# Kernel optimization log

Hardware: AMD Instinct MI355X
Metric: run time of the kernel (lower is better)

The kernel has to match this reference:

```python
import jax, jax.numpy as jnp
import numpy as np

M, K, L, OUT = 16, 64, 6, 128
IN_CH = 2 + 1 + 1 + 1 + 4 * L  # 29
HID_IN = 128 * 2 + 4           # 260


def setup_inputs() -> dict:
    key = jax.random.key(0)
    ks = jax.random.split(key, 5)
    N = 2_000_000
    P = jax.random.normal(ks[0], (N, 2), jnp.float32) * 2.0
    def lin(k, i, o):
        return jax.random.normal(k, (i, o), jnp.float32) / np.float32(np.sqrt(i))
    return {
        'P': P,
        'W1': lin(ks[1], IN_CH, 64), 'b1': jnp.zeros((64,), jnp.float32),
        'W2': lin(ks[2], 64, 128),   'b2': jnp.zeros((128,), jnp.float32),
        'W3': lin(ks[3], HID_IN, 128), 'b3': jnp.zeros((128,), jnp.float32),
        'W4': lin(ks[4], 128, OUT),  'b4': jnp.zeros((OUT,), jnp.float32),
    }


def _fps(P, m):
    # furthest point sampling, seeded at index 0 (standard convention)
    N = P.shape[0]
    def step(carry, _):
        min_d, last_idx = carry
        last = P[last_idx]
        d = jnp.sum((P - last) ** 2, axis=-1)          # [N]
        min_d = jnp.minimum(min_d, d)
        nxt = jnp.argmax(min_d)
        return (min_d, nxt), last_idx
    init = (jnp.full((N,), jnp.finfo(jnp.float32).max, jnp.float32), jnp.int32(0))
    (_, _), idxs = jax.lax.scan(step, init, None, length=m)
    return idxs  # [m] int


def _gelu(x):
    return jax.nn.gelu(x, approximate=False)  # torch nn.GELU default = erf


def reference(P, W1, b1, W2, b2, W3, b3, W4, b4):
    c_idx = jax.lax.stop_gradient(_fps(P, M))
    C = P[c_idx]                                       # [M,2]
    # brute-force kNN: expanded squared distance avoids [M,N,2] intermediate
    Ps = jax.lax.stop_gradient(P)
    Cs = jax.lax.stop_gradient(C)
    d2 = (jnp.sum(Ps ** 2, -1)[None, :]
          - 2.0 * Cs @ Ps.T
          + jnp.sum(Cs ** 2, -1)[:, None])             # [M,N]
    _, nidx = jax.lax.top_k(-d2, K)                    # [M,K]
    patch = P[nidx]                                    # [M,K,2]
    delta = patch - C[:, None, :]                      # [M,K,2]
    r = jnp.linalg.norm(delta, axis=-1, keepdims=True) # [M,K,1]
    theta = jnp.arctan2(delta[..., 1:2], delta[..., 0:1])
    freqs = (2.0 ** jnp.arange(L)).astype(jnp.float32) # [L]
    ang = delta[..., None, :] * freqs[:, None]         # [M,K,L,2]
    ff = jnp.concatenate([jnp.sin(ang), jnp.cos(ang)], -1).reshape(M, K, 4 * L)
    per_pt = jnp.concatenate([delta, r, jnp.sin(theta), jnp.cos(theta), ff], -1)  # [M,K,29]
    h = _gelu(per_pt @ W1 + b1)
    h = _gelu(h @ W2 + b2)                             # [M,K,128]
    h_max = h.max(axis=1)
    h_mean = h.mean(axis=1)
    rr = r[..., 0]                                     # [M,K]
    stats = jnp.stack([rr.mean(1), rr.max(1), rr.min(1), rr.std(1, ddof=1)], -1)  # [M,4]
    z = jnp.concatenate([h_max, h_mean, stats], -1)    # [M,260]
    F = _gelu(z @ W3 + b3) @ W4 + b4                   # [M,OUT]
    return F, C
```

## Files before the change

### kernel.cpp

```cpp
#include <hip/hip_runtime.h>
#include <math.h>

#define MCENT 16
#define KNN   64
#define NBINS 512
#define CAP   7936
#define FPSB  512
#define FPST  256

__device__ __forceinline__ float gelu_f(float x){
    return 0.5f * x * (1.0f + erff(x * 0.70710678118654752440f));
}

__global__ void init_kernel(unsigned int* __restrict__ ghist,
                            unsigned int* __restrict__ cnt){
    const int T = gridDim.x * blockDim.x;
    int t = blockIdx.x * blockDim.x + threadIdx.x;
    for (int i = t; i < MCENT*NBINS; i += T) ghist[i] = 0u;
    if (t < MCENT) cnt[t] = 0u;
}

__global__ __launch_bounds__(FPST) void fps_step(
    const float* __restrict__ P, int N,
    float* __restrict__ min_d,
    unsigned long long* __restrict__ partials,
    int k,
    float* __restrict__ cxy,
    float* __restrict__ outC)
{
    const int lane = threadIdx.x & 63;
    const int wid  = threadIdx.x >> 6;
    __shared__ unsigned long long wred[FPST/64];
    __shared__ int s_cur;

    int cur = 0;
    if (k > 0){
        unsigned long long pb = 0ULL;
        for (int i = threadIdx.x; i < FPSB; i += FPST){
            unsigned long long v = partials[(k-1)*FPSB + i];
            if (v > pb) pb = v;
        }
#pragma unroll
        for (int off = 32; off > 0; off >>= 1){
            unsigned long long o = __shfl_xor(pb, off, 64);
            if (o > pb) pb = o;
        }
        if (lane == 0) wred[wid] = pb;
        __syncthreads();
        if (threadIdx.x == 0){
            unsigned long long b = wred[0];
#pragma unroll
            for (int w = 1; w < FPST/64; ++w) if (wred[w] > b) b = wred[w];
            s_cur = (int)(0xFFFFFFFFu - (unsigned)(b & 0xFFFFFFFFu));
        }
        __syncthreads();
        cur = s_cur;
    }

    if (blockIdx.x == 0 && threadIdx.x == 0){
        float cx = P[2*cur], cy = P[2*cur+1];
        cxy[2*k] = cx; cxy[2*k+1] = cy;
        outC[2*k] = cx; outC[2*k+1] = cy;
    }
    if (k >= MCENT-1) return;

    const float cx = P[2*cur], cy = P[2*cur+1];
    unsigned long long bk = 0ULL;
    const int T = gridDim.x * FPST;
    for (int g = blockIdx.x*FPST + threadIdx.x; g < N; g += T){
        float2 p = ((const float2*)P)[g];
        float dx = __fsub_rn(p.x, cx);
        float dy = __fsub_rn(p.y, cy);
        float d  = __fadd_rn(__fmul_rn(dx,dx), __fmul_rn(dy,dy));
        float nm = (k == 0) ? d : fminf(min_d[g], d);
        min_d[g] = nm;
        unsigned long long key =
            ((unsigned long long)__float_as_uint(nm) << 32)
            | (unsigned long long)(0xFFFFFFFFu - (unsigned)g);
        if (key > bk) bk = key;
    }
#pragma unroll
    for (int off = 32; off > 0; off >>= 1){
        unsigned long long o = __shfl_xor(bk, off, 64);
        if (o > bk) bk = o;
    }
    if (lane == 0) wred[wid] = bk;
    __syncthreads();
    if (threadIdx.x == 0){
        unsigned long long b = wred[0];
#pragma unroll
        for (int w = 1; w < FPST/64; ++w) if (wred[w] > b) b = wred[w];
        partials[k*FPSB + blockIdx.x] = b;
    }
}

__global__ __launch_bounds__(256) void hist_kernel(
    const float* __restrict__ P, int N,
    const float* __restrict__ cxy,
    unsigned int* __restrict__ ghist)
{
    __shared__ unsigned int h[MCENT*NBINS];
    __shared__ float scx[MCENT], scy[MCENT], scs2[MCENT];
    for (int i = threadIdx.x; i < MCENT*NBINS; i += blockDim.x) h[i] = 0u;
    if (threadIdx.x < MCENT){
        float a = cxy[2*threadIdx.x], b = cxy[2*threadIdx.x+1];
        scx[threadIdx.x] = a; scy[threadIdx.x] = b;
        scs2[threadIdx.x] = __fadd_rn(__fmul_rn(a,a), __fmul_rn(b,b));
    }
    __syncthreads();
    const int T = gridDim.x * blockDim.x;
    for (int g = blockIdx.x*blockDim.x + threadIdx.x; g < N; g += T){
        float2 p = ((const float2*)P)[g];
        float x = p.x, y = p.y;
        float ps2 = __fadd_rn(__fmul_rn(x,x), __fmul_rn(y,y));
#pragma unroll
        for (int m = 0; m < MCENT; ++m){
            float dot = __fadd_rn(__fmul_rn(scx[m],x), __fmul_rn(scy[m],y));
            float d2  = __fadd_rn(__fsub_rn(ps2, __fmul_rn(2.0f,dot)), scs2[m]);
            unsigned bin = __float_as_uint(fmaxf(d2, 0.0f)) >> 22;
            atomicAdd(&h[m*NBINS + bin], 1u);
        }
    }
    __syncthreads();
    for (int i = threadIdx.x; i < MCENT*NBINS; i += blockDim.x){
        unsigned v = h[i];
        if (v) atomicAdd(&ghist[i], v);
    }
}

__global__ void thr_kernel(const unsigned int* __restrict__ ghist,
                           float* __restrict__ thr){
    int m = threadIdx.x;
    if (m < MCENT){
        unsigned cum = 0; int B = NBINS-1;
        for (int b = 0; b < NBINS; ++b){
            cum += ghist[m*NBINS + b];
            if (cum >= KNN){ B = b; break; }
        }
        thr[m] = __uint_as_float((unsigned)(B+1) << 22);
    }
}

__global__ __launch_bounds__(256) void collect_kernel(
    const float* __restrict__ P, int N,
    const float* __restrict__ cxy,
    const float* __restrict__ thr,
    unsigned int* __restrict__ cnt,
    float* __restrict__ cd2,
    int* __restrict__ cidx)
{
    __shared__ float scx[MCENT], scy[MCENT], scs2[MCENT], sth[MCENT];
    if (threadIdx.x < MCENT){
        float a = cxy[2*threadIdx.x], b = cxy[2*threadIdx.x+1];
        scx[threadIdx.x]=a; scy[threadIdx.x]=b;
        scs2[threadIdx.x]=__fadd_rn(__fmul_rn(a,a),__fmul_rn(b,b));
        sth[threadIdx.x]=thr[threadIdx.x];
    }
    __syncthreads();
    const int T = gridDim.x*blockDim.x;
    for (int g = blockIdx.x*blockDim.x + threadIdx.x; g < N; g += T){
        float2 p = ((const float2*)P)[g];
        float x = p.x, y = p.y;
        float ps2=__fadd_rn(__fmul_rn(x,x),__fmul_rn(y,y));
#pragma unroll
        for (int m=0;m<MCENT;++m){
            float dot=__fadd_rn(__fmul_rn(scx[m],x),__fmul_rn(scy[m],y));
            float d2=__fadd_rn(__fsub_rn(ps2,__fmul_rn(2.0f,dot)),scs2[m]);
            if (fmaxf(d2,0.0f) < sth[m]){
                unsigned p2 = atomicAdd(&cnt[m], 1u);
                if (p2 < CAP){ cd2[m*CAP+p2]=d2; cidx[m*CAP+p2]=g; }
            }
        }
    }
}

__global__ __launch_bounds__(256) void select_kernel(
    const unsigned int* __restrict__ cnt,
    const float* __restrict__ cd2,
    const int* __restrict__ cidx,
    int* __restrict__ nbr)
{
    const int m = blockIdx.x;
    __shared__ unsigned long long keys[CAP];
    unsigned c = cnt[m]; if (c > CAP) c = CAP;
    for (int i = threadIdx.x; i < (int)c; i += 256){
        unsigned u = __float_as_uint(cd2[m*CAP+i]);
        u = (u & 0x80000000u) ? ~u : (u | 0x80000000u);
        keys[i] = ((unsigned long long)u << 32)
                | (unsigned long long)(unsigned)cidx[m*CAP+i];
    }
    __syncthreads();
    for (int i = threadIdx.x; i < (int)c; i += 256){
        unsigned long long ki = keys[i];
        int rank = 0;
        for (int j = 0; j < (int)c; ++j) rank += (keys[j] < ki);
        if (rank < KNN) nbr[m*KNN + rank] = (int)(unsigned)(ki & 0xFFFFFFFFu);
    }
}

__global__ __launch_bounds__(256) void mlp_kernel(
    const float* __restrict__ P,
    const float* __restrict__ cxy,
    const int* __restrict__ nbr,
    const float* __restrict__ W1, const float* __restrict__ b1,
    const float* __restrict__ W2, const float* __restrict__ b2,
    const float* __restrict__ W3, const float* __restrict__ b3,
    const float* __restrict__ W4, const float* __restrict__ b4,
    float* __restrict__ outF)
{
    const int m = blockIdx.x;
    const int tid = threadIdx.x;
    __shared__ float feat[KNN][32];
    __shared__ float h1[KNN][64];
    __shared__ float sW2[64*128];
    __shared__ float pmax[2][128], psum[2][128];
    __shared__ float z[260];
    __shared__ float part[2][128];
    __shared__ float zz[128];

    for (int i = tid; i < 64*128; i += 256) sW2[i] = W2[i];

    const float cx = cxy[2*m], cy = cxy[2*m+1];
    if (tid < KNN){
        int g = nbr[m*KNN + tid];
        float dx = P[2*g]   - cx;
        float dy = P[2*g+1] - cy;
        float r  = sqrtf(dx*dx + dy*dy);
        float th = atan2f(dy, dx);
        feat[tid][0]=dx; feat[tid][1]=dy; feat[tid][2]=r;
        feat[tid][3]=sinf(th); feat[tid][4]=cosf(th);
        float fx = dx, fy = dy;
#pragma unroll
        for (int l = 0; l < 6; ++l){
            feat[tid][5+4*l+0]=sinf(fx);
            feat[tid][5+4*l+1]=sinf(fy);
            feat[tid][5+4*l+2]=cosf(fx);
            feat[tid][5+4*l+3]=cosf(fy);
            fx += fx; fy += fy;
        }
    }
    __syncthreads();

    for (int rep = 0; rep < 16; ++rep){
        int o = rep*256 + tid;
        int k = o >> 6, j = o & 63;
        float acc = b1[j];
#pragma unroll
        for (int c = 0; c < 29; ++c) acc += feat[k][c] * W1[c*64 + j];
        h1[k][j] = gelu_f(acc);
    }
    __syncthreads();

    {
        int j = tid & 127, kh = tid >> 7;
        float lmax = -3.402823466e+38f, lsum = 0.f;
        for (int kk = 0; kk < 32; ++kk){
            int k = kh*32 + kk;
            float acc = b2[j];
#pragma unroll 8
            for (int i = 0; i < 64; ++i) acc += h1[k][i] * sW2[i*128 + j];
            float v = gelu_f(acc);
            lmax = fmaxf(lmax, v);
            lsum += v;
        }
        pmax[kh][j] = lmax; psum[kh][j] = lsum;
    }
    __syncthreads();
    if (tid < 128){
        z[tid]       = fmaxf(pmax[0][tid], pmax[1][tid]);
        z[128 + tid] = (psum[0][tid] + psum[1][tid]) * (1.0f/64.0f);
    }
    if (tid < 64){
        float r = feat[tid][2];
        float s = r, mx = r, mn = r;
        for (int off = 1; off < 64; off <<= 1){
            s  += __shfl_xor(s, off, 64);
            mx  = fmaxf(mx, __shfl_xor(mx, off, 64));
            mn  = fminf(mn, __shfl_xor(mn, off, 64));
        }
        float mean = s * (1.0f/64.0f);
        float dv = (r-mean)*(r-mean);
        for (int off = 1; off < 64; off <<= 1) dv += __shfl_xor(dv, off, 64);
        if (tid == 0){
            z[256]=mean; z[257]=mx; z[258]=mn; z[259]=sqrtf(dv*(1.0f/63.0f));
        }
    }
    __syncthreads();

    {
        int j = tid & 127, half = tid >> 7;
        float acc = 0.f;
        for (int i = half*130; i < half*130+130; ++i) acc += z[i]*W3[i*128+j];
        part[half][j] = acc;
    }
    __syncthreads();
    if (tid < 128) zz[tid] = gelu_f(part[0][tid] + part[1][tid] + b3[tid]);
    __syncthreads();
    {
        int j = tid & 127, half = tid >> 7;
        float acc = 0.f;
        for (int i = half*64; i < half*64+64; ++i) acc += zz[i]*W4[i*128+j];
        part[half][j] = acc;
    }
    __syncthreads();
    if (tid < 128) outF[m*128 + tid] = part[0][tid] + part[1][tid] + b4[tid];
}

extern "C" void kernel_launch(void* const* d_in, const int* in_sizes, int n_in,
                              void* d_out, int out_size, void* d_ws, size_t ws_size,
                              hipStream_t stream)
{
    const float* P  = (const float*)d_in[0];
    const float* W1 = (const float*)d_in[1];
    const float* b1 = (const float*)d_in[2];
    const float* W2 = (const float*)d_in[3];
    const float* b2 = (const float*)d_in[4];
    const float* W3 = (const float*)d_in[5];
    const float* b3 = (const float*)d_in[6];
    const float* W4 = (const float*)d_in[7];
    const float* b4 = (const float*)d_in[8];
    int N = in_sizes[0] / 2;
    float* outF = (float*)d_out;
    float* outC = outF + MCENT*128;
    (void)n_in; (void)out_size; (void)ws_size;

    char* base = (char*)d_ws;
    size_t off = 0;
    auto take = [&](size_t bytes)->char*{
        char* p = base + off;
        off = (off + bytes + 255) & ~(size_t)255;
        return p;
    };
    unsigned long long* partials = (unsigned long long*)take((size_t)MCENT*FPSB*8);
    float* cxy         = (float*)take(MCENT*2*4);
    unsigned int* ghist= (unsigned int*)take(MCENT*NBINS*4);
    unsigned int* cnt  = (unsigned int*)take(MCENT*4);
    float* thr         = (float*)take(MCENT*4);
    int*   nbr         = (int*)  take(MCENT*KNN*4);
    float* cd2         = (float*)take((size_t)MCENT*CAP*4);
    int*   cidx        = (int*)  take((size_t)MCENT*CAP*4);
    float* min_d       = (float*)take((size_t)N*4);

    init_kernel<<<32, 256, 0, stream>>>(ghist, cnt);

    for (int k = 0; k < MCENT-1; ++k)
        fps_step<<<FPSB, FPST, 0, stream>>>(P, N, min_d, partials, k, cxy, outC);
    fps_step<<<1, FPST, 0, stream>>>(P, N, min_d, partials, MCENT-1, cxy, outC);

    hist_kernel<<<512, 256, 0, stream>>>(P, N, cxy, ghist);
    thr_kernel<<<1, 64, 0, stream>>>(ghist, thr);
    collect_kernel<<<512, 256, 0, stream>>>(P, N, cxy, thr, cnt, cd2, cidx);
    select_kernel<<<MCENT, 256, 0, stream>>>(cnt, cd2, cidx, nbr);
    mlp_kernel<<<MCENT, 256, 0, stream>>>(P, cxy, nbr, W1,b1,W2,b2,W3,b3,W4,b4, outF);
}
```

Baseline: 337.4 us.

## Vectorize point loads, fold init into FPS, widen MLP block to 1024 threads

The FPS, histogram and collect kernels now load two points per thread as float4 (and min_d as float2), with a scalar tail for odd N. The histogram and counter zeroing moves into the first FPS step, which removes one launch. The MLP kernel runs with 1024 threads, stages W1 in shared memory and splits the layer-2, W3 and W4 reductions over 8 segments, cutting the serial work per thread in this small 16-block kernel. The risks are more shared-memory atomic pressure per iteration and fewer points per thread to hide latency.

```diff
diff --git a/kernel.cpp b/kernel.cpp
--- a/kernel.cpp
+++ b/kernel.cpp
@@ -7,17 +7,10 @@
 #define CAP   7936
 #define FPSB  512
 #define FPST  256
+#define MLPT  1024
 
 __device__ __forceinline__ float gelu_f(float x){
     return 0.5f * x * (1.0f + erff(x * 0.70710678118654752440f));
-}
-
-__global__ void init_kernel(unsigned int* __restrict__ ghist,
-                            unsigned int* __restrict__ cnt){
-    const int T = gridDim.x * blockDim.x;
-    int t = blockIdx.x * blockDim.x + threadIdx.x;
-    for (int i = t; i < MCENT*NBINS; i += T) ghist[i] = 0u;
-    if (t < MCENT) cnt[t] = 0u;
 }
 
 __global__ __launch_bounds__(FPST) void fps_step(
@@ -26,12 +19,20 @@
     unsigned long long* __restrict__ partials,
     int k,
     float* __restrict__ cxy,
-    float* __restrict__ outC)
+    float* __restrict__ outC,
+    unsigned int* __restrict__ ghist,
+    unsigned int* __restrict__ cnt)
 {
     const int lane = threadIdx.x & 63;
     const int wid  = threadIdx.x >> 6;
     __shared__ unsigned long long wred[FPST/64];
     __shared__ int s_cur;
+
+    if (k == 0){
+        int gi = blockIdx.x*FPST + threadIdx.x;
+        if (gi < MCENT*NBINS) ghist[gi] = 0u;
+        if (gi < MCENT) cnt[gi] = 0u;
+    }
 
     int cur = 0;
     if (k > 0){
@@ -66,18 +67,41 @@
 
     const float cx = P[2*cur], cy = P[2*cur+1];
     unsigned long long bk = 0ULL;
-    const int T = gridDim.x * FPST;
-    for (int g = blockIdx.x*FPST + threadIdx.x; g < N; g += T){
-        float2 p = ((const float2*)P)[g];
-        float dx = __fsub_rn(p.x, cx);
-        float dy = __fsub_rn(p.y, cy);
+    const int T  = gridDim.x * FPST;
+    const int NP = N >> 1;
+    for (int q = blockIdx.x*FPST + threadIdx.x; q < NP; q += T){
+        float4 p = ((const float4*)P)[q];
+        float dx0 = __fsub_rn(p.x, cx), dy0 = __fsub_rn(p.y, cy);
+        float d0  = __fadd_rn(__fmul_rn(dx0,dx0), __fmul_rn(dy0,dy0));
+        float dx1 = __fsub_rn(p.z, cx), dy1 = __fsub_rn(p.w, cy);
+        float d1  = __fadd_rn(__fmul_rn(dx1,dx1), __fmul_rn(dy1,dy1));
+        float2 mp;
+        if (k == 0){ mp.x = d0; mp.y = d1; }
+        else {
+            mp = ((const float2*)min_d)[q];
+            mp.x = fminf(mp.x, d0); mp.y = fminf(mp.y, d1);
+        }
+        ((float2*)min_d)[q] = mp;
+        int g = 2*q;
+        unsigned long long k0 =
+            ((unsigned long long)__float_as_uint(mp.x) << 32)
+            | (unsigned long long)(0xFFFFFFFFu - (unsigned)g);
+        unsigned long long k1 =
+            ((unsigned long long)__float_as_uint(mp.y) << 32)
+            | (unsigned long long)(0xFFFFFFFFu - (unsigned)(g+1));
+        if (k0 > bk) bk = k0;
+        if (k1 > bk) bk = k1;
+    }
+    if ((N & 1) && blockIdx.x == 0 && threadIdx.x == 0){
+        int g = N-1;
+        float dx = __fsub_rn(P[2*g], cx), dy = __fsub_rn(P[2*g+1], cy);
         float d  = __fadd_rn(__fmul_rn(dx,dx), __fmul_rn(dy,dy));
         float nm = (k == 0) ? d : fminf(min_d[g], d);
         min_d[g] = nm;
-        unsigned long long key =
+        unsigned long long kk =
             ((unsigned long long)__float_as_uint(nm) << 32)
             | (unsigned long long)(0xFFFFFFFFu - (unsigned)g);
-        if (key > bk) bk = key;
+        if (kk > bk) bk = kk;
     }
 #pragma unroll
     for (int off = 32; off > 0; off >>= 1){
@@ -108,17 +132,29 @@
         scs2[threadIdx.x] = __fadd_rn(__fmul_rn(a,a), __fmul_rn(b,b));
     }
     __syncthreads();
-    const int T = gridDim.x * blockDim.x;
-    for (int g = blockIdx.x*blockDim.x + threadIdx.x; g < N; g += T){
-        float2 p = ((const float2*)P)[g];
-        float x = p.x, y = p.y;
+    const int T  = gridDim.x * blockDim.x;
+    const int NP = N >> 1;
+    for (int q = blockIdx.x*blockDim.x + threadIdx.x; q < NP; q += T){
+        float4 p = ((const float4*)P)[q];
+        float ps20 = __fadd_rn(__fmul_rn(p.x,p.x), __fmul_rn(p.y,p.y));
+        float ps21 = __fadd_rn(__fmul_rn(p.z,p.z), __fmul_rn(p.w,p.w));
+#pragma unroll
+        for (int m = 0; m < MCENT; ++m){
+            float dot0 = __fadd_rn(__fmul_rn(scx[m],p.x), __fmul_rn(scy[m],p.y));
+            float d20  = __fadd_rn(__fsub_rn(ps20, __fmul_rn(2.0f,dot0)), scs2[m]);
+            atomicAdd(&h[m*NBINS + (__float_as_uint(fmaxf(d20,0.0f)) >> 22)], 1u);
+            float dot1 = __fadd_rn(__fmul_rn(scx[m],p.z), __fmul_rn(scy[m],p.w));
+            float d21  = __fadd_rn(__fsub_rn(ps21, __fmul_rn(2.0f,dot1)), scs2[m]);
+            atomicAdd(&h[m*NBINS + (__float_as_uint(fmaxf(d21,0.0f)) >> 22)], 1u);
+        }
+    }
+    if ((N & 1) && blockIdx.x == 0 && threadIdx.x == 0){
+        float x = P[2*(N-1)], y = P[2*(N-1)+1];
         float ps2 = __fadd_rn(__fmul_rn(x,x), __fmul_rn(y,y));
-#pragma unroll
         for (int m = 0; m < MCENT; ++m){
             float dot = __fadd_rn(__fmul_rn(scx[m],x), __fmul_rn(scy[m],y));
             float d2  = __fadd_rn(__fsub_rn(ps2, __fmul_rn(2.0f,dot)), scs2[m]);
-            unsigned bin = __float_as_uint(fmaxf(d2, 0.0f)) >> 22;
-            atomicAdd(&h[m*NBINS + bin], 1u);
+            atomicAdd(&h[m*NBINS + (__float_as_uint(fmaxf(d2,0.0f)) >> 22)], 1u);
         }
     }
     __syncthreads();
@@ -157,18 +193,39 @@
         sth[threadIdx.x]=thr[threadIdx.x];
     }
     __syncthreads();
-    const int T = gridDim.x*blockDim.x;
-    for (int g = blockIdx.x*blockDim.x + threadIdx.x; g < N; g += T){
-        float2 p = ((const float2*)P)[g];
-        float x = p.x, y = p.y;
-        float ps2=__fadd_rn(__fmul_rn(x,x),__fmul_rn(y,y));
-#pragma unroll
-        for (int m=0;m<MCENT;++m){
-            float dot=__fadd_rn(__fmul_rn(scx[m],x),__fmul_rn(scy[m],y));
-            float d2=__fadd_rn(__fsub_rn(ps2,__fmul_rn(2.0f,dot)),scs2[m]);
+    const int T  = gridDim.x*blockDim.x;
+    const int NP = N >> 1;
+    for (int q = blockIdx.x*blockDim.x + threadIdx.x; q < NP; q += T){
+        float4 p = ((const float4*)P)[q];
+        float ps20 = __fadd_rn(__fmul_rn(p.x,p.x), __fmul_rn(p.y,p.y));
+        float ps21 = __fadd_rn(__fmul_rn(p.z,p.z), __fmul_rn(p.w,p.w));
+        int g = 2*q;
+#pragma unroll
+        for (int m = 0; m < MCENT; ++m){
+            float dot0 = __fadd_rn(__fmul_rn(scx[m],p.x), __fmul_rn(scy[m],p.y));
+            float d20  = __fadd_rn(__fsub_rn(ps20, __fmul_rn(2.0f,dot0)), scs2[m]);
+            if (fmaxf(d20,0.0f) < sth[m]){
+                unsigned pos = atomicAdd(&cnt[m], 1u);
+                if (pos < CAP){ cd2[m*CAP+pos]=d20; cidx[m*CAP+pos]=g; }
+            }
+            float dot1 = __fadd_rn(__fmul_rn(scx[m],p.z), __fmul_rn(scy[m],p.w));
+            float d21  = __fadd_rn(__fsub_rn(ps21, __fmul_rn(2.0f,dot1)), scs2[m]);
+            if (fmaxf(d21,0.0f) < sth[m]){
+                unsigned pos = atomicAdd(&cnt[m], 1u);
+                if (pos < CAP){ cd2[m*CAP+pos]=d21; cidx[m*CAP+pos]=g+1; }
+            }
+        }
+    }
+    if ((N & 1) && blockIdx.x == 0 && threadIdx.x == 0){
+        int g = N-1;
+        float x = P[2*g], y = P[2*g+1];
+        float ps2 = __fadd_rn(__fmul_rn(x,x), __fmul_rn(y,y));
+        for (int m = 0; m < MCENT; ++m){
+            float dot = __fadd_rn(__fmul_rn(scx[m],x), __fmul_rn(scy[m],y));
+            float d2  = __fadd_rn(__fsub_rn(ps2, __fmul_rn(2.0f,dot)), scs2[m]);
             if (fmaxf(d2,0.0f) < sth[m]){
-                unsigned p2 = atomicAdd(&cnt[m], 1u);
-                if (p2 < CAP){ cd2[m*CAP+p2]=d2; cidx[m*CAP+p2]=g; }
+                unsigned pos = atomicAdd(&cnt[m], 1u);
+                if (pos < CAP){ cd2[m*CAP+pos]=d2; cidx[m*CAP+pos]=g; }
             }
         }
     }
@@ -198,7 +255,7 @@
     }
 }
 
-__global__ __launch_bounds__(256) void mlp_kernel(
+__global__ __launch_bounds__(MLPT) void mlp_kernel(
     const float* __restrict__ P,
     const float* __restrict__ cxy,
     const int* __restrict__ nbr,
@@ -211,14 +268,21 @@
     const int m = blockIdx.x;
     const int tid = threadIdx.x;
     __shared__ float feat[KNN][32];
-    __shared__ float h1[KNN][64];
+    __shared__ float h1s[KNN][64];
+    __shared__ float sW1[29*64];
     __shared__ float sW2[64*128];
-    __shared__ float pmax[2][128], psum[2][128];
+    __shared__ float pmax[8][128], psum[8][128];
     __shared__ float z[260];
-    __shared__ float part[2][128];
+    __shared__ float part[8][128];
     __shared__ float zz[128];
 
-    for (int i = tid; i < 64*128; i += 256) sW2[i] = W2[i];
+    {
+        const float4* s2 = (const float4*)W2;
+        float4* d2 = (float4*)sW2;
+        d2[tid]        = s2[tid];
+        d2[tid + 1024] = s2[tid + 1024];
+        if (tid < 464) ((float4*)sW1)[tid] = ((const float4*)W1)[tid];
+    }
 
     const float cx = cxy[2*m], cy = cxy[2*m+1];
     if (tid < KNN){
@@ -241,24 +305,25 @@
     }
     __syncthreads();
 
-    for (int rep = 0; rep < 16; ++rep){
-        int o = rep*256 + tid;
+#pragma unroll
+    for (int rep = 0; rep < 4; ++rep){
+        int o = rep*MLPT + tid;
         int k = o >> 6, j = o & 63;
         float acc = b1[j];
 #pragma unroll
-        for (int c = 0; c < 29; ++c) acc += feat[k][c] * W1[c*64 + j];
-        h1[k][j] = gelu_f(acc);
+        for (int c = 0; c < 29; ++c) acc += feat[k][c] * sW1[c*64 + j];
+        h1s[k][j] = gelu_f(acc);
     }
     __syncthreads();
 
     {
         int j = tid & 127, kh = tid >> 7;
         float lmax = -3.402823466e+38f, lsum = 0.f;
-        for (int kk = 0; kk < 32; ++kk){
-            int k = kh*32 + kk;
+        for (int kk = 0; kk < 8; ++kk){
+            int k = kh*8 + kk;
             float acc = b2[j];
 #pragma unroll 8
-            for (int i = 0; i < 64; ++i) acc += h1[k][i] * sW2[i*128 + j];
+            for (int i = 0; i < 64; ++i) acc += h1s[k][i] * sW2[i*128 + j];
             float v = gelu_f(acc);
             lmax = fmaxf(lmax, v);
             lsum += v;
@@ -267,11 +332,15 @@
     }
     __syncthreads();
     if (tid < 128){
-        z[tid]       = fmaxf(pmax[0][tid], pmax[1][tid]);
-        z[128 + tid] = (psum[0][tid] + psum[1][tid]) * (1.0f/64.0f);
-    }
-    if (tid < 64){
-        float r = feat[tid][2];
+        float mx = pmax[0][tid], sm = psum[0][tid];
+#pragma unroll
+        for (int w = 1; w < 8; ++w){ mx = fmaxf(mx, pmax[w][tid]); sm += psum[w][tid]; }
+        z[tid]       = mx;
+        z[128 + tid] = sm * (1.0f/64.0f);
+    }
+    if (tid >= 128 && tid < 192){
+        int l = tid - 128;
+        float r = feat[l][2];
         float s = r, mx = r, mn = r;
         for (int off = 1; off < 64; off <<= 1){
             s  += __shfl_xor(s, off, 64);
@@ -281,29 +350,42 @@
         float mean = s * (1.0f/64.0f);
         float dv = (r-mean)*(r-mean);
         for (int off = 1; off < 64; off <<= 1) dv += __shfl_xor(dv, off, 64);
-        if (tid == 0){
+        if (l == 0){
             z[256]=mean; z[257]=mx; z[258]=mn; z[259]=sqrtf(dv*(1.0f/63.0f));
         }
     }
     __syncthreads();
 
     {
-        int j = tid & 127, half = tid >> 7;
+        int j = tid & 127, seg = tid >> 7;
+        int i0  = (seg < 4) ? seg*33 : 132 + (seg-4)*32;
+        int cnt = (seg < 4) ? 33 : 32;
         float acc = 0.f;
-        for (int i = half*130; i < half*130+130; ++i) acc += z[i]*W3[i*128+j];
-        part[half][j] = acc;
-    }
-    __syncthreads();
-    if (tid < 128) zz[tid] = gelu_f(part[0][tid] + part[1][tid] + b3[tid]);
+        for (int i = i0; i < i0 + cnt; ++i) acc += z[i]*W3[i*128+j];
+        part[seg][j] = acc;
+    }
+    __syncthreads();
+    if (tid < 128){
+        float a = part[0][tid];
+#pragma unroll
+        for (int w = 1; w < 8; ++w) a += part[w][tid];
+        zz[tid] = gelu_f(a + b3[tid]);
+    }
     __syncthreads();
     {
-        int j = tid & 127, half = tid >> 7;
+        int j = tid & 127, seg = tid >> 7;
         float acc = 0.f;
-        for (int i = half*64; i < half*64+64; ++i) acc += zz[i]*W4[i*128+j];
-        part[half][j] = acc;
-    }
-    __syncthreads();
-    if (tid < 128) outF[m*128 + tid] = part[0][tid] + part[1][tid] + b4[tid];
+#pragma unroll
+        for (int i = seg*16; i < seg*16+16; ++i) acc += zz[i]*W4[i*128+j];
+        part[seg][j] = acc;
+    }
+    __syncthreads();
+    if (tid < 128){
+        float a = part[0][tid];
+#pragma unroll
+        for (int w = 1; w < 8; ++w) a += part[w][tid];
+        outF[m*128 + tid] = a + b4[tid];
+    }
 }
 
 extern "C" void kernel_launch(void* const* d_in, const int* in_sizes, int n_in,
@@ -341,15 +423,15 @@
     int*   cidx        = (int*)  take((size_t)MCENT*CAP*4);
     float* min_d       = (float*)take((size_t)N*4);
 
-    init_kernel<<<32, 256, 0, stream>>>(ghist, cnt);
-
     for (int k = 0; k < MCENT-1; ++k)
-        fps_step<<<FPSB, FPST, 0, stream>>>(P, N, min_d, partials, k, cxy, outC);
-    fps_step<<<1, FPST, 0, stream>>>(P, N, min_d, partials, MCENT-1, cxy, outC);
+        fps_step<<<FPSB, FPST, 0, stream>>>(P, N, min_d, partials, k, cxy, outC,
+                                            ghist, cnt);
+    fps_step<<<1, FPST, 0, stream>>>(P, N, min_d, partials, MCENT-1, cxy, outC,
+                                     ghist, cnt);
 
     hist_kernel<<<512, 256, 0, stream>>>(P, N, cxy, ghist);
     thr_kernel<<<1, 64, 0, stream>>>(ghist, thr);
     collect_kernel<<<512, 256, 0, stream>>>(P, N, cxy, thr, cnt, cd2, cidx);
     select_kernel<<<MCENT, 256, 0, stream>>>(cnt, cd2, cidx, nbr);
-    mlp_kernel<<<MCENT, 256, 0, stream>>>(P, cxy, nbr, W1,b1,W2,b2,W3,b3,W4,b4, outF);
-}
+    mlp_kernel<<<MCENT, MLPT, 0, stream>>>(P, cxy, nbr, W1,b1,W2,b2,W3,b3,W4,b4, outF);
+}
```

Result: faster. 310.6 us (-7.9%).
